# Performance work log

Measured on AMD Instinct MI355X. Metric: run time of the kernel, lower is better.

## Reference

```python
import jax, jax.numpy as jnp
import numpy as np

B, T, D, H = 2, 2048, 1024, 16
HD = D // H


def sinusoidal_rel_pe(seq_len, d_model, dtype=jnp.float32):
    # Relative positions T-1 .. 0 (reversed), standard sin/cos interleave.
    pos = jnp.arange(seq_len - 1, -1, -1, dtype=jnp.float32)[:, None]  # [T,1]
    div = jnp.exp(-jnp.log(jnp.float32(10000.0)) * jnp.arange(0, d_model, 2, dtype=jnp.float32) / d_model)
    pe = jnp.zeros((seq_len, d_model), dtype=jnp.float32)
    pe = pe.at[:, 0::2].set(jnp.sin(pos * div))
    pe = pe.at[:, 1::2].set(jnp.cos(pos * div))
    return pe.astype(dtype)


def relative_to_absolute(x):
    # x: [B,H,T,L] with L == T. Music-Transformer skew trick.
    b, h, t1, l = x.shape
    x = jnp.pad(x, ((0, 0), (0, 0), (0, 0), (1, 0)))          # pad left of last dim
    x = x.reshape(b, h, -1)
    x = jnp.pad(x, ((0, 0), (0, 0), (l - t1, 0)))
    x = x.reshape(b, h, 1 + t1, l)
    return x[:, :, 1:]


def setup_inputs() -> dict:
    key = jax.random.key(0)
    k1, k2, k3 = jax.random.split(key, 3)
    x = jax.random.normal(k1, (B, T, D), dtype=jnp.float32)
    # causal mask: True where attention is disallowed (j > i)
    mask = jnp.triu(jnp.ones((T, T), dtype=bool), k=1)[None, None]
    mask = jnp.broadcast_to(mask, (B, 1, T, T))
    Wqkv = jax.random.normal(k2, (D, 3 * D), dtype=jnp.float32) * 0.02
    Wout = jax.random.normal(k3, (D, D), dtype=jnp.float32) * 0.02
    bout = jnp.zeros((D,), dtype=jnp.float32)
    return {"x": x, "mask": mask, "Wqkv": Wqkv, "Wout": Wout, "bout": bout}


def reference(x, mask, Wqkv, Wout, bout):
    b, t, d = x.shape
    scale = jnp.sqrt(jnp.float32(HD)).astype(x.dtype)
    qkv = x @ Wqkv                                  # [B,T,3D]
    q, k, v = jnp.split(qkv, 3, axis=-1)
    E = sinusoidal_rel_pe(t, d, x.dtype)            # [T,D], constant rel bias
    q = q.reshape(b, t, H, HD).transpose(0, 2, 1, 3)   # [B,H,T,hd]
    k = k.reshape(b, t, H, HD).transpose(0, 2, 1, 3)
    v = v.reshape(b, t, H, HD).transpose(0, 2, 1, 3)
    Eh = E.reshape(t, H, HD).transpose(1, 0, 2)        # [H,T,hd]
    att_k = jnp.einsum('bhqd,bhkd->bhqk', q, k)
    att_e = relative_to_absolute(jnp.einsum('bhqd,hkd->bhqk', q, Eh))
    score = (att_k + att_e) / scale
    score = jnp.where(mask, -jnp.inf, score)
    score = jax.nn.softmax(score, axis=-1)          # dropout is identity (eval)
    ctx = jnp.einsum('bhqk,bhkd->bhqd', score, v)
    ctx = ctx.transpose(0, 2, 1, 3).reshape(b, t, d)
    out = ctx @ Wout + bout
    return (out, score)
```

## Files before the change

### kernel.cpp

```cpp
#include <hip/hip_runtime.h>

typedef __bf16 bf16x8 __attribute__((ext_vector_type(8)));
typedef float f32x4 __attribute__((ext_vector_type(4)));
typedef float f32x16 __attribute__((ext_vector_type(16)));

#define B_ 2
#define T_ 2048
#define D_ 1024
#define H_ 16

__device__ __forceinline__ ushort f2bf(float f) {
  union { float f; unsigned u; } v; v.f = f;
  unsigned u = v.u;
  return (ushort)((u + 0x7FFFu + ((u >> 16) & 1u)) >> 16);
}
__device__ __forceinline__ float b2f(ushort u) {
  union { unsigned u; float f; } v; v.u = ((unsigned)u) << 16;
  return v.f;
}

__device__ __forceinline__ void g2l16(const void* g, void* l) {
  __builtin_amdgcn_global_load_lds(
      (const __attribute__((address_space(1))) unsigned int*)g,
      (__attribute__((address_space(3))) unsigned int*)l, 16, 0, 0);
}

__global__ __launch_bounds__(256) void cvt_kernel(const float* __restrict__ in,
                                                  ushort* __restrict__ out) {
  int i = (blockIdx.x * 256 + threadIdx.x) * 4;
  float4 v = *(const float4*)(in + i);
  ushort4 o;
  o.x = f2bf(v.x); o.y = f2bf(v.y); o.z = f2bf(v.z); o.w = f2bf(v.w);
  *(ushort4*)(out + i) = o;
}

__global__ void transpose_cvt(const float* __restrict__ in, ushort* __restrict__ out,
                              int R, int C) {
  __shared__ float tile[32][33];
  int bx = blockIdx.x * 32, by = blockIdx.y * 32;
  int tx = threadIdx.x, ty = threadIdx.y;
  for (int i = 0; i < 32; i += 8)
    tile[ty + i][tx] = in[(size_t)(by + ty + i) * C + (bx + tx)];
  __syncthreads();
  for (int i = 0; i < 32; i += 8)
    out[(size_t)(bx + ty + i) * R + (by + tx)] = f2bf(tile[tx][ty + i]);
}

__global__ __launch_bounds__(256) void gemm_bf16(
    const ushort* __restrict__ A, const ushort* __restrict__ BT,
    float* __restrict__ C, const float* __restrict__ bias,
    int M, int N, int K) {
  __shared__ alignas(16) ushort As[2][4096];
  __shared__ alignas(16) ushort Bs[2][4096];
  int tid = threadIdx.x;
  int wave = tid >> 6, lane = tid & 63;
  int l16 = lane & 15, lhi = lane >> 4;
  int m0 = blockIdx.y * 128, n0 = blockIdx.x * 128;
  int wr = (wave >> 1) * 64, wc = (wave & 1) * 64;
  int srow = lane >> 2, sch = lane & 3;

  f32x4 acc[4][4] = {};

  auto stage = [&](int kk, int buf) {
    for (int i = 0; i < 2; ++i) {
      int rg = i * 4 + wave;
      g2l16(A + (size_t)(m0 + rg * 16 + srow) * K + kk + sch * 8, &As[buf][rg * 512]);
      g2l16(BT + (size_t)(n0 + rg * 16 + srow) * K + kk + sch * 8, &Bs[buf][rg * 512]);
    }
  };

  stage(0, 0);
  int buf = 0;
  for (int kk = 0; kk < K; kk += 32) {
    __syncthreads();
    if (kk + 32 < K) stage(kk + 32, buf ^ 1);
    const ushort* Asb = As[buf];
    const ushort* Bsb = Bs[buf];
    bf16x8 af[4], bfr[4];
    for (int f = 0; f < 4; ++f)
      af[f] = *(const bf16x8*)(Asb + (wr + f * 16 + l16) * 32 + lhi * 8);
    for (int f = 0; f < 4; ++f)
      bfr[f] = *(const bf16x8*)(Bsb + (wc + f * 16 + l16) * 32 + lhi * 8);
    for (int fm = 0; fm < 4; ++fm)
      for (int fn = 0; fn < 4; ++fn)
        acc[fm][fn] = __builtin_amdgcn_mfma_f32_16x16x32_bf16(af[fm], bfr[fn], acc[fm][fn], 0, 0, 0);
    buf ^= 1;
  }
  for (int fm = 0; fm < 4; ++fm)
    for (int fn = 0; fn < 4; ++fn)
      for (int r = 0; r < 4; ++r) {
        int row = m0 + wr + fm * 16 + lhi * 4 + r;
        int col = n0 + wc + fn * 16 + l16;
        float v = acc[fm][fn][r];
        if (bias) v += bias[col];
        C[(size_t)row * N + col] = v;
      }
}

__global__ __launch_bounds__(256) void gemm_bf16_ob(
    const ushort* __restrict__ A, const ushort* __restrict__ BT,
    ushort* __restrict__ C, int M, int N, int K) {
  __shared__ alignas(16) ushort As[2][4096];
  __shared__ alignas(16) ushort Bs[2][4096];
  int tid = threadIdx.x;
  int wave = tid >> 6, lane = tid & 63;
  int l16 = lane & 15, lhi = lane >> 4;
  int m0 = blockIdx.y * 128, n0 = blockIdx.x * 128;
  int wr = (wave >> 1) * 64, wc = (wave & 1) * 64;
  int srow = lane >> 2, sch = lane & 3;

  f32x4 acc[4][4] = {};

  auto stage = [&](int kk, int buf) {
    for (int i = 0; i < 2; ++i) {
      int rg = i * 4 + wave;
      g2l16(A + (size_t)(m0 + rg * 16 + srow) * K + kk + sch * 8, &As[buf][rg * 512]);
      g2l16(BT + (size_t)(n0 + rg * 16 + srow) * K + kk + sch * 8, &Bs[buf][rg * 512]);
    }
  };

  stage(0, 0);
  int buf = 0;
  for (int kk = 0; kk < K; kk += 32) {
    __syncthreads();
    if (kk + 32 < K) stage(kk + 32, buf ^ 1);
    const ushort* Asb = As[buf];
    const ushort* Bsb = Bs[buf];
    bf16x8 af[4], bfr[4];
    for (int f = 0; f < 4; ++f)
      af[f] = *(const bf16x8*)(Asb + (wr + f * 16 + l16) * 32 + lhi * 8);
    for (int f = 0; f < 4; ++f)
      bfr[f] = *(const bf16x8*)(Bsb + (wc + f * 16 + l16) * 32 + lhi * 8);
    for (int fm = 0; fm < 4; ++fm)
      for (int fn = 0; fn < 4; ++fn)
        acc[fm][fn] = __builtin_amdgcn_mfma_f32_16x16x32_bf16(af[fm], bfr[fn], acc[fm][fn], 0, 0, 0);
    buf ^= 1;
  }
  for (int fm = 0; fm < 4; ++fm)
    for (int fn = 0; fn < 4; ++fn)
      for (int r = 0; r < 4; ++r) {
        int row = m0 + wr + fm * 16 + lhi * 4 + r;
        int col = n0 + wc + fn * 16 + l16;
        C[(size_t)row * N + col] = f2bf(acc[fm][fn][r]);
      }
}

__global__ __launch_bounds__(256) void augment_kernel(
    const ushort* __restrict__ qkvb,
    ushort* __restrict__ Qaug, ushort* __restrict__ Kaug, ushort* __restrict__ Vb) {
  int row = blockIdx.x;
  int b = row >> 11;
  int t = row & 2047;
  int tid = threadIdx.x;
  const ushort* src = qkvb + (size_t)row * 3072;

  {
    int d4 = tid * 4;
    int h = d4 >> 6, d = d4 & 63;
    size_t obase = ((size_t)(b * H_ + h) * T_ + t);
    ushort4 q = *(const ushort4*)(src + d4);
    ushort4 k = *(const ushort4*)(src + 1024 + d4);
    ushort4 v = *(const ushort4*)(src + 2048 + d4);
    ushort4 qs;
    qs.x = f2bf(b2f(q.x) * 0.125f); qs.y = f2bf(b2f(q.y) * 0.125f);
    qs.z = f2bf(b2f(q.z) * 0.125f); qs.w = f2bf(b2f(q.w) * 0.125f);
    *(ushort4*)(Qaug + obase * 128 + d) = qs;
    *(ushort4*)(Kaug + obase * 128 + d) = k;
    *(ushort4*)(Vb + obase * 64 + d) = v;
  }
  for (int i = 0; i < 2; ++i) {
    int idx = tid + i * 256;
    int h = idx >> 5, mm = idx & 31;
    int gdim = h * 64 + 2 * mm;
    float w = __expf(-9.2103403719761836f * (float)gdim * (1.0f / 1024.0f));
    float ang = w * (float)t;
    float si, co;
    __sincosf(ang, &si, &co);
    ushort2 qp = *(const ushort2*)(src + h * 64 + 2 * mm);
    float qs = b2f(qp.x), qc = b2f(qp.y);
    size_t obase = ((size_t)(b * H_ + h) * T_ + t);
    ushort2 qo, ko;
    qo.x = f2bf((qs * si + qc * co) * 0.125f);
    qo.y = f2bf((qc * si - qs * co) * 0.125f);
    ko.x = f2bf(co);
    ko.y = f2bf(si);
    *(ushort2*)(Qaug + obase * 128 + 64 + 2 * mm) = qo;
    *(ushort2*)(Kaug + obase * 128 + 64 + 2 * mm) = ko;
  }
}

__global__ __launch_bounds__(256) void transpose_v(const ushort* __restrict__ Vb,
                                                   ushort* __restrict__ Vt) {
  __shared__ ushort tile[64][72];
  int bh = blockIdx.y, t0 = blockIdx.x * 64;
  int tid = threadIdx.x;
  for (int i = 0; i < 2; ++i) {
    int e = tid + i * 256;
    int row = e >> 3, ch = e & 7;
    *(int4*)(&tile[row][ch * 8]) =
        *(const int4*)(Vb + ((size_t)bh * T_ + t0 + row) * 64 + ch * 8);
  }
  __syncthreads();
  for (int i = 0; i < 2; ++i) {
    int e = tid + i * 256;
    int d = e >> 3, ch = e & 7;
    union { int4 v; ushort u[8]; } pk;
    for (int u = 0; u < 8; ++u) pk.u[u] = tile[ch * 8 + u][d];
    *(int4*)(Vt + ((size_t)bh * 64 + d) * T_ + t0 + ch * 8) = pk.v;
  }
}

__device__ __forceinline__ int rowf32(int reg, int hi) {
  return (reg & 3) + 8 * (reg >> 2) + 4 * hi;
}

__global__ __launch_bounds__(256, 4) void denom_kernel(
    const ushort* __restrict__ Qaug,
    const ushort* __restrict__ Kaug,
    float* __restrict__ invlb) {
  int flat = blockIdx.y * 32 + blockIdx.x;
  int wg = (flat & 7) * 128 + (flat >> 3);
  int bh = wg >> 5;
  int qt = 31 - (wg & 31);
  int tid = threadIdx.x;
  int wave = tid >> 6, lane = tid & 63;
  int l31 = lane & 31, hi = lane >> 5;
  int r = wave >> 1, d = wave & 1;

  __shared__ alignas(16) ushort Ks[2][8192];
  __shared__ float sums[64];

  const ushort* Kbase = Kaug + (size_t)bh * T_ * 128;

  auto stageK = [&](int kt, int buf) {
    for (int i = 0; i < 4; ++i) {
      int rg = i * 4 + wave;
      int key = rg * 4 + (lane >> 4);
      const ushort* g = Kbase + ((size_t)(kt * 64 + key)) * 128 + (((lane & 15) ^ (key & 15)) << 3);
      g2l16(g, &Ks[buf][rg * 512]);
    }
  };

  bf16x8 qf[8];
  {
    const ushort* Qg = Qaug + ((size_t)bh * T_ + qt * 64 + r * 32 + l31) * 128;
    for (int ks = 0; ks < 8; ++ks)
      qf[ks] = *(const bf16x8*)(Qg + ks * 16 + hi * 8);
  }
  int key = d * 32 + l31;

  stageK(0, 0);
  asm volatile("s_waitcnt vmcnt(0)" ::: "memory");
  __builtin_amdgcn_s_barrier();
  float plsum[16];
  for (int i = 0; i < 16; ++i) plsum[i] = 0.f;

  for (int kt = 0; kt <= qt; ++kt) {
    int buf = kt & 1;
    if (kt < qt) stageK(kt + 1, buf ^ 1);
    __builtin_amdgcn_sched_barrier(0);
    const ushort* Kb = Ks[buf];
    f32x16 s = {};
    for (int ks = 0; ks < 8; ++ks) {
      int slot = (ks * 2 + hi) ^ (key & 15);
      bf16x8 kf = *(const bf16x8*)(Kb + key * 128 + (slot << 3));
      s = __builtin_amdgcn_mfma_f32_32x32x16_bf16(qf[ks], kf, s, 0, 0, 0);
    }
    if (kt == qt) {
      for (int reg = 0; reg < 16; ++reg)
        if (d * 32 + l31 > r * 32 + rowf32(reg, hi)) s[reg] = -1e30f;
    }
    for (int reg = 0; reg < 16; ++reg) plsum[reg] += __expf(s[reg]);
    if (kt < qt) {
      asm volatile("s_waitcnt vmcnt(0)" ::: "memory");
      __builtin_amdgcn_s_barrier();
    }
  }
  for (int reg = 0; reg < 16; ++reg) {
    float v = plsum[reg];
    for (int dd = 1; dd < 32; dd <<= 1) v += __shfl_xor(v, dd);
    plsum[reg] = v;
  }
  if (d == 1 && l31 == 0)
    for (int reg = 0; reg < 16; ++reg)
      sums[r * 32 + rowf32(reg, hi)] = plsum[reg];
  __syncthreads();
  if (d == 0 && l31 == 0)
    for (int reg = 0; reg < 16; ++reg) {
      int row = r * 32 + rowf32(reg, hi);
      invlb[(size_t)bh * T_ + qt * 64 + row] = 1.f / (plsum[reg] + sums[row]);
    }
}

__global__ __launch_bounds__(256) void attn2_kernel(
    const ushort* __restrict__ Qaug,
    const ushort* __restrict__ Kaug,
    const ushort* __restrict__ Vt,
    const float* __restrict__ invlb,
    float* __restrict__ score,
    ushort* __restrict__ ctxb) {
  int flat = blockIdx.y * 32 + blockIdx.x;
  int wg = (flat & 7) * 128 + (flat >> 3);
  int bh = wg >> 5;
  int qt = 31 - (wg & 31);
  int tid = threadIdx.x;
  int wave = tid >> 6, lane = tid & 63;
  int l31 = lane & 31, hi = lane >> 5;
  int r = wave >> 1, d = wave & 1;

  __shared__ alignas(16) ushort Ks[2][8192];
  __shared__ alignas(16) ushort Vs[2][4096];
  __shared__ alignas(16) ushort Ps[4096];

  const ushort* Kbase = Kaug + (size_t)bh * T_ * 128;
  const ushort* Vbase = Vt + (size_t)bh * 64 * T_;

  auto stageK = [&](int kt, int buf) {
    for (int i = 0; i < 4; ++i) {
      int rg = i * 4 + wave;
      int key = rg * 4 + (lane >> 4);
      const ushort* g = Kbase + ((size_t)(kt * 64 + key)) * 128 + (((lane & 15) ^ (key & 15)) << 3);
      g2l16(g, &Ks[buf][rg * 512]);
    }
  };
  auto stageV = [&](int kt, int buf) {
    for (int i = 0; i < 2; ++i) {
      int rg = i * 4 + wave;
      int dim = rg * 8 + (lane >> 3);
      const ushort* g = Vbase + (size_t)dim * T_ + kt * 64 + (((lane & 7) ^ (dim & 7)) << 3);
      g2l16(g, &Vs[buf][rg * 512]);
    }
  };

  bf16x8 qf[8];
  {
    const ushort* Qg = Qaug + ((size_t)bh * T_ + qt * 64 + r * 32 + l31) * 128;
    for (int ks = 0; ks < 8; ++ks)
      qf[ks] = *(const bf16x8*)(Qg + ks * 16 + hi * 8);
  }
  int key = d * 32 + l31;
  float4 iv[4];
  for (int g = 0; g < 4; ++g)
    iv[g] = *(const float4*)(invlb + (size_t)bh * T_ + qt * 64 + r * 32 + hi * 4 + g * 8);

  stageK(0, 0);
  stageV(0, 0);
  asm volatile("s_waitcnt vmcnt(0)" ::: "memory");
  __builtin_amdgcn_s_barrier();
  f32x16 cacc[2] = {};
  float* srow = score + ((size_t)bh * T_ + (size_t)qt * 64) * T_;

  for (int kt = 0; kt <= qt; ++kt) {
    int buf = kt & 1;
    if (kt < qt) { stageK(kt + 1, buf ^ 1); stageV(kt + 1, buf ^ 1); }
    __builtin_amdgcn_sched_barrier(0);
    const ushort* Kb = Ks[buf];
    f32x16 s = {};
    for (int ks = 0; ks < 8; ++ks) {
      int slot = (ks * 2 + hi) ^ (key & 15);
      bf16x8 kf = *(const bf16x8*)(Kb + key * 128 + (slot << 3));
      s = __builtin_amdgcn_mfma_f32_32x32x16_bf16(qf[ks], kf, s, 0, 0, 0);
    }
    if (kt == qt) {
      for (int reg = 0; reg < 16; ++reg)
        if (d * 32 + l31 > r * 32 + rowf32(reg, hi)) s[reg] = -1e30f;
    }
    for (int reg = 0; reg < 16; ++reg) {
      int row_loc = r * 32 + rowf32(reg, hi);
      float p = __expf(s[reg]) * iv[reg >> 2][reg & 3];
      srow[(size_t)row_loc * T_ + kt * 64 + key] = p;
      Ps[row_loc * 64 + ((((key >> 3)) ^ (row_loc & 7)) << 3) + (key & 7)] = f2bf(p);
    }
    asm volatile("s_waitcnt lgkmcnt(0)" ::: "memory");
    __builtin_amdgcn_sched_barrier(0);
    const ushort* Vb2 = Vs[buf];
    int rowA = r * 32 + l31;
    for (int ks2 = 0; ks2 < 2; ++ks2) {
      int chunkA = d * 4 + ks2 * 2 + hi;
      bf16x8 pa = *(const bf16x8*)(Ps + rowA * 64 + ((chunkA ^ (rowA & 7)) << 3));
      for (int b2 = 0; b2 < 2; ++b2) {
        int dim = b2 * 32 + l31;
        bf16x8 vb = *(const bf16x8*)(Vb2 + dim * 64 + ((chunkA ^ (dim & 7)) << 3));
        cacc[b2] = __builtin_amdgcn_mfma_f32_32x32x16_bf16(pa, vb, cacc[b2], 0, 0, 0);
      }
    }
    if (kt < qt) {
      asm volatile("s_waitcnt vmcnt(16)" ::: "memory");
      __builtin_amdgcn_s_barrier();
    }
  }

  {
    int row = tid >> 2, c16 = (tid & 3) * 16;
    f32x4 z = {0.f, 0.f, 0.f, 0.f};
    for (int kt = qt + 1; kt < 32; ++kt) {
      f32x4* dst = (f32x4*)(srow + (size_t)row * T_ + kt * 64 + c16);
      for (int u = 0; u < 4; ++u) dst[u] = z;
    }
  }

  __builtin_amdgcn_s_barrier();
  float* xch = (float*)Ks;
  if (d == 1) {
    for (int b2 = 0; b2 < 2; ++b2)
      for (int reg = 0; reg < 16; ++reg)
        xch[(r * 32 + rowf32(reg, hi)) * 64 + b2 * 32 + l31] = cacc[b2][reg];
  }
  __syncthreads();
  if (d == 0) {
    int b = bh >> 4, h = bh & 15;
    for (int b2 = 0; b2 < 2; ++b2)
      for (int reg = 0; reg < 16; ++reg) {
        int row_loc = r * 32 + rowf32(reg, hi);
        float v = cacc[b2][reg] + xch[row_loc * 64 + b2 * 32 + l31];
        int t = qt * 64 + row_loc;
        ctxb[((size_t)(b * T_ + t)) * 1024 + h * 64 + b2 * 32 + l31] = f2bf(v);
      }
  }
}

extern "C" void kernel_launch(void* const* d_in, const int* in_sizes, int n_in,
                              void* d_out, int out_size, void* d_ws, size_t ws_size,
                              hipStream_t stream) {
  const float* x    = (const float*)d_in[0];
  const float* Wqkv = (const float*)d_in[2];
  const float* Wout = (const float*)d_in[3];
  const float* bout = (const float*)d_in[4];

  char* ws = (char*)d_ws;
  ushort* xb    = (ushort*)(ws + 0);
  ushort* wqkvT = (ushort*)(ws + 8388608);
  ushort* woutT = (ushort*)(ws + 14680064);
  ushort* qkvb  = (ushort*)(ws + 16777216);
  ushort* Qaug  = (ushort*)(ws + 50331648);
  ushort* Kaug  = (ushort*)(ws + 67108864);
  ushort* Vb    = (ushort*)(ws + 83886080);
  ushort* Vt    = (ushort*)(ws + 92274688);
  ushort* ctxb  = (ushort*)(ws + 100663296);
  float*  invlb = (float*) (ws + 109051904);

  float* out   = (float*)d_out;
  float* score = out + (size_t)4194304;

  cvt_kernel<<<4096, 256, 0, stream>>>(x, xb);
  dim3 tb(32, 8);
  transpose_cvt<<<dim3(3072 / 32, 1024 / 32), tb, 0, stream>>>(Wqkv, wqkvT, 1024, 3072);
  transpose_cvt<<<dim3(1024 / 32, 1024 / 32), tb, 0, stream>>>(Wout, woutT, 1024, 1024);
  gemm_bf16_ob<<<dim3(24, 32), 256, 0, stream>>>(xb, wqkvT, qkvb, 4096, 3072, 1024);
  augment_kernel<<<4096, 256, 0, stream>>>(qkvb, Qaug, Kaug, Vb);
  transpose_v<<<dim3(32, 32), 256, 0, stream>>>(Vb, Vt);
  denom_kernel<<<dim3(32, 32), 256, 0, stream>>>(Qaug, Kaug, invlb);
  attn2_kernel<<<dim3(32, 32), 256, 0, stream>>>(Qaug, Kaug, Vt, invlb, score, ctxb);
  gemm_bf16<<<dim3(8, 32), 256, 0, stream>>>(ctxb, woutT, out, bout, 4096, 1024, 1024);
}
```

Measured before the change: 314.7 us.

## Fuse denominator and attention passes by buffering full score rows in LDS

```diff
diff --git a/kernel.cpp b/kernel.cpp
--- a/kernel.cpp
+++ b/kernel.cpp
@@ -2,7 +2,6 @@
 
 typedef __bf16 bf16x8 __attribute__((ext_vector_type(8)));
 typedef float f32x4 __attribute__((ext_vector_type(4)));
-typedef float f32x16 __attribute__((ext_vector_type(16)));
 
 #define B_ 2
 #define T_ 2048
@@ -210,212 +209,165 @@
   }
 }
 
-__device__ __forceinline__ int rowf32(int reg, int hi) {
-  return (reg & 3) + 8 * (reg >> 2) + 4 * hi;
-}
-
-__global__ __launch_bounds__(256, 4) void denom_kernel(
+__global__ __launch_bounds__(256, 2) void attn_sbuf(
     const ushort* __restrict__ Qaug,
     const ushort* __restrict__ Kaug,
-    float* __restrict__ invlb) {
-  int flat = blockIdx.y * 32 + blockIdx.x;
-  int wg = (flat & 7) * 128 + (flat >> 3);
-  int bh = wg >> 5;
-  int qt = 31 - (wg & 31);
+    const ushort* __restrict__ Vt,
+    float* __restrict__ score,
+    ushort* __restrict__ ctxb) {
+  extern __shared__ char dynsmem[];
+  ushort* Sbuf  = (ushort*)dynsmem;
+  ushort* Ktile = (ushort*)(dynsmem + 65536);
+  ushort* Vtile = (ushort*)(dynsmem + 65536);
+  float*  sc    = (float*)(dynsmem + 65536 + 8192);
+
+  int flat = blockIdx.y * 128 + blockIdx.x;
+  int wg = (flat & 7) * 512 + (flat >> 3);
+  int bh = wg >> 7;
+  int qt = 127 - (wg & 127);
+  int qrow0 = qt * 16;
+  int klim = qt >> 2;
+
   int tid = threadIdx.x;
   int wave = tid >> 6, lane = tid & 63;
-  int l31 = lane & 31, hi = lane >> 5;
-  int r = wave >> 1, d = wave & 1;
-
-  __shared__ alignas(16) ushort Ks[2][8192];
-  __shared__ float sums[64];
+  int l16 = lane & 15, lhi = lane >> 4, e7 = l16 & 7;
 
   const ushort* Kbase = Kaug + (size_t)bh * T_ * 128;
-
-  auto stageK = [&](int kt, int buf) {
+  const ushort* Vbase = Vt + (size_t)bh * 64 * T_;
+
+  bf16x8 qf[4];
+  {
+    const ushort* Qg = Qaug + ((size_t)bh * T_ + qrow0 + l16) * 128;
+    for (int ks = 0; ks < 4; ++ks)
+      qf[ks] = *(const bf16x8*)(Qg + ks * 32 + lhi * 8);
+  }
+
+  int4 kreg[4];
+  auto loadK = [&](int kt) {
+#pragma unroll
     for (int i = 0; i < 4; ++i) {
       int rg = i * 4 + wave;
       int key = rg * 4 + (lane >> 4);
-      const ushort* g = Kbase + ((size_t)(kt * 64 + key)) * 128 + (((lane & 15) ^ (key & 15)) << 3);
-      g2l16(g, &Ks[buf][rg * 512]);
-    }
-  };
-
-  bf16x8 qf[8];
-  {
-    const ushort* Qg = Qaug + ((size_t)bh * T_ + qt * 64 + r * 32 + l31) * 128;
-    for (int ks = 0; ks < 8; ++ks)
-      qf[ks] = *(const bf16x8*)(Qg + ks * 16 + hi * 8);
-  }
-  int key = d * 32 + l31;
-
-  stageK(0, 0);
-  asm volatile("s_waitcnt vmcnt(0)" ::: "memory");
-  __builtin_amdgcn_s_barrier();
-  float plsum[16];
-  for (int i = 0; i < 16; ++i) plsum[i] = 0.f;
-
-  for (int kt = 0; kt <= qt; ++kt) {
-    int buf = kt & 1;
-    if (kt < qt) stageK(kt + 1, buf ^ 1);
+      kreg[i] = *(const int4*)(Kbase + ((size_t)(kt * 64 + key)) * 128 +
+                               (((lane & 15) ^ (key & 7)) << 3));
+    }
+  };
+  auto writeK = [&]() {
+#pragma unroll
+    for (int i = 0; i < 4; ++i)
+      *(int4*)(Ktile + (i * 4 + wave) * 512 + lane * 8) = kreg[i];
+  };
+
+  loadK(0);
+  writeK();
+  __syncthreads();
+  float plsum[4] = {0.f, 0.f, 0.f, 0.f};
+  int keyloc = wave * 16 + l16;
+  for (int kt = 0; kt <= klim; ++kt) {
+    if (kt < klim) loadK(kt + 1);
     __builtin_amdgcn_sched_barrier(0);
-    const ushort* Kb = Ks[buf];
-    f32x16 s = {};
-    for (int ks = 0; ks < 8; ++ks) {
-      int slot = (ks * 2 + hi) ^ (key & 15);
-      bf16x8 kf = *(const bf16x8*)(Kb + key * 128 + (slot << 3));
-      s = __builtin_amdgcn_mfma_f32_32x32x16_bf16(qf[ks], kf, s, 0, 0, 0);
-    }
-    if (kt == qt) {
-      for (int reg = 0; reg < 16; ++reg)
-        if (d * 32 + l31 > r * 32 + rowf32(reg, hi)) s[reg] = -1e30f;
-    }
-    for (int reg = 0; reg < 16; ++reg) plsum[reg] += __expf(s[reg]);
-    if (kt < qt) {
-      asm volatile("s_waitcnt vmcnt(0)" ::: "memory");
-      __builtin_amdgcn_s_barrier();
-    }
-  }
-  for (int reg = 0; reg < 16; ++reg) {
-    float v = plsum[reg];
-    for (int dd = 1; dd < 32; dd <<= 1) v += __shfl_xor(v, dd);
-    plsum[reg] = v;
-  }
-  if (d == 1 && l31 == 0)
-    for (int reg = 0; reg < 16; ++reg)
-      sums[r * 32 + rowf32(reg, hi)] = plsum[reg];
-  __syncthreads();
-  if (d == 0 && l31 == 0)
-    for (int reg = 0; reg < 16; ++reg) {
-      int row = r * 32 + rowf32(reg, hi);
-      invlb[(size_t)bh * T_ + qt * 64 + row] = 1.f / (plsum[reg] + sums[row]);
-    }
-}
-
-__global__ __launch_bounds__(256) void attn2_kernel(
-    const ushort* __restrict__ Qaug,
-    const ushort* __restrict__ Kaug,
-    const ushort* __restrict__ Vt,
-    const float* __restrict__ invlb,
-    float* __restrict__ score,
-    ushort* __restrict__ ctxb) {
-  int flat = blockIdx.y * 32 + blockIdx.x;
-  int wg = (flat & 7) * 128 + (flat >> 3);
-  int bh = wg >> 5;
-  int qt = 31 - (wg & 31);
-  int tid = threadIdx.x;
-  int wave = tid >> 6, lane = tid & 63;
-  int l31 = lane & 31, hi = lane >> 5;
-  int r = wave >> 1, d = wave & 1;
-
-  __shared__ alignas(16) ushort Ks[2][8192];
-  __shared__ alignas(16) ushort Vs[2][4096];
-  __shared__ alignas(16) ushort Ps[4096];
-
-  const ushort* Kbase = Kaug + (size_t)bh * T_ * 128;
-  const ushort* Vbase = Vt + (size_t)bh * 64 * T_;
-
-  auto stageK = [&](int kt, int buf) {
-    for (int i = 0; i < 4; ++i) {
-      int rg = i * 4 + wave;
-      int key = rg * 4 + (lane >> 4);
-      const ushort* g = Kbase + ((size_t)(kt * 64 + key)) * 128 + (((lane & 15) ^ (key & 15)) << 3);
-      g2l16(g, &Ks[buf][rg * 512]);
-    }
-  };
-  auto stageV = [&](int kt, int buf) {
+    f32x4 s = {};
+#pragma unroll
+    for (int ks = 0; ks < 4; ++ks) {
+      int slot = (ks * 4 + lhi) ^ e7;
+      bf16x8 kf = *(const bf16x8*)(Ktile + keyloc * 128 + (slot << 3));
+      s = __builtin_amdgcn_mfma_f32_16x16x32_bf16(qf[ks], kf, s, 0, 0, 0);
+    }
+    if (kt == klim) {
+      for (int r = 0; r < 4; ++r)
+        if (kt * 64 + keyloc > qrow0 + lhi * 4 + r) s[r] = -1e30f;
+    }
+    for (int r = 0; r < 4; ++r) {
+      float p = __expf(s[r]);
+      plsum[r] += p;
+      int row_loc = lhi * 4 + r;
+      int col = kt * 64 + keyloc;
+      Sbuf[row_loc * 2048 + (((col >> 3) ^ (row_loc & 7)) << 3) + (col & 7)] = f2bf(p);
+    }
+    if (kt < klim) {
+      __syncthreads();
+      writeK();
+      __syncthreads();
+    }
+  }
+  for (int r = 0; r < 4; ++r)
+    for (int dd = 1; dd < 16; dd <<= 1)
+      plsum[r] += __shfl_xor(plsum[r], dd);
+  __syncthreads();
+  if (l16 == 0)
+    for (int r = 0; r < 4; ++r)
+      sc[wave * 16 + lhi * 4 + r] = plsum[r];
+  __syncthreads();
+
+  int4 vreg[2];
+  auto loadV = [&](int kt) {
+#pragma unroll
     for (int i = 0; i < 2; ++i) {
       int rg = i * 4 + wave;
       int dim = rg * 8 + (lane >> 3);
-      const ushort* g = Vbase + (size_t)dim * T_ + kt * 64 + (((lane & 7) ^ (dim & 7)) << 3);
-      g2l16(g, &Vs[buf][rg * 512]);
-    }
-  };
-
-  bf16x8 qf[8];
+      vreg[i] = *(const int4*)(Vbase + (size_t)dim * T_ + kt * 64 +
+                               (((lane & 7) ^ (dim & 7)) << 3));
+    }
+  };
+  auto writeV = [&]() {
+#pragma unroll
+    for (int i = 0; i < 2; ++i)
+      *(int4*)(Vtile + (i * 4 + wave) * 512 + lane * 8) = vreg[i];
+  };
+  loadV(0);
+  writeV();
+  __syncthreads();
+  f32x4 cacc = {};
+  int dimloc = wave * 16 + l16;
+  for (int kt = 0; kt <= klim; ++kt) {
+    if (kt < klim) loadV(kt + 1);
+    __builtin_amdgcn_sched_barrier(0);
+#pragma unroll
+    for (int ks2 = 0; ks2 < 2; ++ks2) {
+      int pslot = (kt * 8 + ks2 * 4 + lhi) ^ e7;
+      bf16x8 pa = *(const bf16x8*)(Sbuf + l16 * 2048 + (pslot << 3));
+      int vslot = (ks2 * 4 + lhi) ^ e7;
+      bf16x8 vb = *(const bf16x8*)(Vtile + dimloc * 64 + (vslot << 3));
+      cacc = __builtin_amdgcn_mfma_f32_16x16x32_bf16(pa, vb, cacc, 0, 0, 0);
+    }
+    if (kt < klim) {
+      __syncthreads();
+      writeV();
+      __syncthreads();
+    }
+  }
+
   {
-    const ushort* Qg = Qaug + ((size_t)bh * T_ + qt * 64 + r * 32 + l31) * 128;
-    for (int ks = 0; ks < 8; ++ks)
-      qf[ks] = *(const bf16x8*)(Qg + ks * 16 + hi * 8);
-  }
-  int key = d * 32 + l31;
-  float4 iv[4];
-  for (int g = 0; g < 4; ++g)
-    iv[g] = *(const float4*)(invlb + (size_t)bh * T_ + qt * 64 + r * 32 + hi * 4 + g * 8);
-
-  stageK(0, 0);
-  stageV(0, 0);
-  asm volatile("s_waitcnt vmcnt(0)" ::: "memory");
-  __builtin_amdgcn_s_barrier();
-  f32x16 cacc[2] = {};
-  float* srow = score + ((size_t)bh * T_ + (size_t)qt * 64) * T_;
-
-  for (int kt = 0; kt <= qt; ++kt) {
-    int buf = kt & 1;
-    if (kt < qt) { stageK(kt + 1, buf ^ 1); stageV(kt + 1, buf ^ 1); }
-    __builtin_amdgcn_sched_barrier(0);
-    const ushort* Kb = Ks[buf];
-    f32x16 s = {};
-    for (int ks = 0; ks < 8; ++ks) {
-      int slot = (ks * 2 + hi) ^ (key & 15);
-      bf16x8 kf = *(const bf16x8*)(Kb + key * 128 + (slot << 3));
-      s = __builtin_amdgcn_mfma_f32_32x32x16_bf16(qf[ks], kf, s, 0, 0, 0);
-    }
-    if (kt == qt) {
-      for (int reg = 0; reg < 16; ++reg)
-        if (d * 32 + l31 > r * 32 + rowf32(reg, hi)) s[reg] = -1e30f;
-    }
-    for (int reg = 0; reg < 16; ++reg) {
-      int row_loc = r * 32 + rowf32(reg, hi);
-      float p = __expf(s[reg]) * iv[reg >> 2][reg & 3];
-      srow[(size_t)row_loc * T_ + kt * 64 + key] = p;
-      Ps[row_loc * 64 + ((((key >> 3)) ^ (row_loc & 7)) << 3) + (key & 7)] = f2bf(p);
-    }
-    asm volatile("s_waitcnt lgkmcnt(0)" ::: "memory");
-    __builtin_amdgcn_sched_barrier(0);
-    const ushort* Vb2 = Vs[buf];
-    int rowA = r * 32 + l31;
-    for (int ks2 = 0; ks2 < 2; ++ks2) {
-      int chunkA = d * 4 + ks2 * 2 + hi;
-      bf16x8 pa = *(const bf16x8*)(Ps + rowA * 64 + ((chunkA ^ (rowA & 7)) << 3));
-      for (int b2 = 0; b2 < 2; ++b2) {
-        int dim = b2 * 32 + l31;
-        bf16x8 vb = *(const bf16x8*)(Vb2 + dim * 64 + ((chunkA ^ (dim & 7)) << 3));
-        cacc[b2] = __builtin_amdgcn_mfma_f32_32x32x16_bf16(pa, vb, cacc[b2], 0, 0, 0);
+    int bb = bh >> 4, hh = bh & 15;
+    for (int r = 0; r < 4; ++r) {
+      int row = lhi * 4 + r;
+      float invr = 1.f / (sc[row] + sc[16 + row] + sc[32 + row] + sc[48 + row]);
+      int t = qrow0 + row;
+      ctxb[((size_t)(bb * T_ + t)) * 1024 + hh * 64 + dimloc] = f2bf(cacc[r] * invr);
+    }
+  }
+
+  float* srow = score + ((size_t)bh * T_ + qrow0) * T_;
+  int lim = (klim + 1) * 64;
+  for (int rr = 0; rr < 4; ++rr) {
+    int row = wave * 4 + rr;
+    float invr = 1.f / (sc[row] + sc[16 + row] + sc[32 + row] + sc[48 + row]);
+    float* dst = srow + (size_t)row * T_;
+    for (int it = 0; it < 4; ++it) {
+      int c = lane + it * 64;
+      int c0 = c * 8;
+      f32x4 lo = {0.f, 0.f, 0.f, 0.f}, hi = {0.f, 0.f, 0.f, 0.f};
+      if (c0 < lim) {
+        int4 u = *(const int4*)(Sbuf + row * 2048 + ((c ^ (row & 7)) << 3));
+        const ushort* us = (const ushort*)&u;
+        lo[0] = b2f(us[0]) * invr; lo[1] = b2f(us[1]) * invr;
+        lo[2] = b2f(us[2]) * invr; lo[3] = b2f(us[3]) * invr;
+        hi[0] = b2f(us[4]) * invr; hi[1] = b2f(us[5]) * invr;
+        hi[2] = b2f(us[6]) * invr; hi[3] = b2f(us[7]) * invr;
       }
-    }
-    if (kt < qt) {
-      asm volatile("s_waitcnt vmcnt(16)" ::: "memory");
-      __builtin_amdgcn_s_barrier();
-    }
-  }
-
-  {
-    int row = tid >> 2, c16 = (tid & 3) * 16;
-    f32x4 z = {0.f, 0.f, 0.f, 0.f};
-    for (int kt = qt + 1; kt < 32; ++kt) {
-      f32x4* dst = (f32x4*)(srow + (size_t)row * T_ + kt * 64 + c16);
-      for (int u = 0; u < 4; ++u) dst[u] = z;
-    }
-  }
-
-  __builtin_amdgcn_s_barrier();
-  float* xch = (float*)Ks;
-  if (d == 1) {
-    for (int b2 = 0; b2 < 2; ++b2)
-      for (int reg = 0; reg < 16; ++reg)
-        xch[(r * 32 + rowf32(reg, hi)) * 64 + b2 * 32 + l31] = cacc[b2][reg];
-  }
-  __syncthreads();
-  if (d == 0) {
-    int b = bh >> 4, h = bh & 15;
-    for (int b2 = 0; b2 < 2; ++b2)
-      for (int reg = 0; reg < 16; ++reg) {
-        int row_loc = r * 32 + rowf32(reg, hi);
-        float v = cacc[b2][reg] + xch[row_loc * 64 + b2 * 32 + l31];
-        int t = qt * 64 + row_loc;
-        ctxb[((size_t)(b * T_ + t)) * 1024 + h * 64 + b2 * 32 + l31] = f2bf(v);
-      }
+      *(f32x4*)(dst + c0) = lo;
+      *(f32x4*)(dst + c0 + 4) = hi;
+    }
   }
 }
 
@@ -437,10 +389,14 @@
   ushort* Vb    = (ushort*)(ws + 83886080);
   ushort* Vt    = (ushort*)(ws + 92274688);
   ushort* ctxb  = (ushort*)(ws + 100663296);
-  float*  invlb = (float*) (ws + 109051904);
 
   float* out   = (float*)d_out;
   float* score = out + (size_t)4194304;
+
+  static bool attr_set = false;
+  (void)attr_set;
+  hipFuncSetAttribute((const void*)attn_sbuf,
+                      hipFuncAttributeMaxDynamicSharedMemorySize, 81920);
 
   cvt_kernel<<<4096, 256, 0, stream>>>(x, xb);
   dim3 tb(32, 8);
@@ -449,7 +405,6 @@
   gemm_bf16_ob<<<dim3(24, 32), 256, 0, stream>>>(xb, wqkvT, qkvb, 4096, 3072, 1024);
   augment_kernel<<<4096, 256, 0, stream>>>(qkvb, Qaug, Kaug, Vb);
   transpose_v<<<dim3(32, 32), 256, 0, stream>>>(Vb, Vt);
-  denom_kernel<<<dim3(32, 32), 256, 0, stream>>>(Qaug, Kaug, invlb);
-  attn2_kernel<<<dim3(32, 32), 256, 0, stream>>>(Qaug, Kaug, Vt, invlb, score, ctxb);
+  attn_sbuf<<<dim3(128, 32), 256, 81920, stream>>>(Qaug, Kaug, Vt, score, ctxb);
   gemm_bf16<<<dim3(8, 32), 256, 0, stream>>>(ctxb, woutT, out, bout, 4096, 1024, 1024);
 }
```

Result: slower. 583.6 us (+85.5%).
